# Optimization experiments

Measured on AMD Instinct MI355X. Metric: run time of the kernel, lower is better.

## Reference

```python
import jax, jax.numpy as jnp
import numpy as np
from jax import lax

WIN = 11
SIGMA = 1.5
C1 = 0.01 ** 2
C2 = 0.03 ** 2


def _gauss_window(c):
    x = np.arange(WIN) - WIN // 2
    g = np.exp(-(x ** 2) / (2.0 * SIGMA ** 2))
    g = g / g.sum()
    w2d = np.outer(g, g).astype(np.float32)  # [11,11]
    return jnp.asarray(np.broadcast_to(w2d, (c, 1, WIN, WIN)).copy())


def _dwconv(x, kernel, groups):
    # x: [B,C,H,W], kernel: [C,1,kh,kw] depthwise, stride 1, SAME padding
    return lax.conv_general_dilated(
        x, kernel, window_strides=(1, 1), padding='SAME',
        dimension_numbers=('NCHW', 'OIHW', 'NCHW'),
        feature_group_count=groups)


_SOBEL_X = jnp.asarray(np.array([[-1, 0, 1], [-2, 0, 2], [-1, 0, 1]], np.float32))
_SOBEL_Y = jnp.asarray(np.array([[1, 2, 1], [0, 0, 0], [-1, -2, -1]], np.float32))


def _sobel_xy(x):
    # x: [B,3,H,W] -> depthwise 3x3 sobel on each channel (same as per-channel conv2d)
    c = x.shape[1]
    kx = jnp.broadcast_to(_SOBEL_X, (c, 1, 3, 3))
    ky = jnp.broadcast_to(_SOBEL_Y, (c, 1, 3, 3))
    return _dwconv(x, kx, c), _dwconv(x, ky, c)


def _rgb2ycrcb(im):
    R, G, B = im[:, 0:1], im[:, 1:2], im[:, 2:3]
    Y = 0.299 * R + 0.587 * G + 0.114 * B
    Cr = (R - Y) * 0.713 + 0.5
    Cb = (B - Y) * 0.564 + 0.5
    return Y, Cr, Cb


def _ssim(img1, img2, channel):
    w = _gauss_window(channel)
    mu1 = _dwconv(img1, w, channel)
    mu2 = _dwconv(img2, w, channel)
    mu1_sq = mu1 * mu1
    mu2_sq = mu2 * mu2
    mu12 = mu1 * mu2
    s1 = _dwconv(img1 * img1, w, channel) - mu1_sq
    s2 = _dwconv(img2 * img2, w, channel) - mu2_sq
    s12 = _dwconv(img1 * img2, w, channel) - mu12
    ssim_map = ((2 * mu12 + C1) * (2 * s12 + C2)) / ((mu1_sq + mu2_sq + C1) * (s1 + s2 + C2))
    return ssim_map.mean()


def _l1(a, b):
    return jnp.mean(jnp.abs(a - b))


def setup_inputs() -> dict:
    key = jax.random.key(0)
    k1, k2, k3 = jax.random.split(key, 3)
    shp = (16, 3, 512, 512)
    return {
        'input_vis': jax.random.uniform(k1, shp, jnp.float32),
        'input_ir': jax.random.uniform(k2, shp, jnp.float32),
        'fuse': jax.random.uniform(k3, shp, jnp.float32),
    }


def reference(input_vis, input_ir, fuse):
    # color components
    _, Cr_F, Cb_F = _rgb2ycrcb(fuse)
    _, Cr_V, Cb_V = _rgb2ycrcb(input_vis)
    Y_ir = input_ir[:, 0:1]

    # sobel gradients (depthwise over 3 channels == per-channel conv + cat)
    Fgx, Fgy = _sobel_xy(fuse)
    Vgx, Vgy = _sobel_xy(input_vis)
    Igx, Igy = _sobel_xy(input_ir)
    joint_gx = jnp.maximum(Vgx, Igx)
    joint_gy = jnp.maximum(Vgy, Igy)
    joint_int = jnp.maximum(input_vis, input_ir)

    con_loss = _l1(fuse, joint_int)
    gradient_loss = 0.5 * _l1(Fgx, joint_gx) + 0.5 * _l1(Fgy, joint_gy)
    color_loss = _l1(Cb_F, Cb_V) + _l1(Cr_F, Cr_V)

    # SSIM: rgb-vs-fused (3ch) and ir-Y vs gray(fused) (1ch)
    ssim_rgb = _ssim(input_vis, fuse, 3)
    gray_fused = (0.2989 * fuse[:, 0:1] + 0.587 * fuse[:, 1:2] + 0.114 * fuse[:, 2:3])
    ssim_ir = _ssim(Y_ir, gray_fused, 1)
    ssim_loss = 1.0 - (ssim_rgb + ssim_ir) / 2.0

    return 0.5 * con_loss + 0.2 * gradient_loss + 1.0 * color_loss + 0.1 * ssim_loss
```

## Files before the change

kernel.cpp:

```cpp
#include <hip/hip_runtime.h>

#define IMG_H 512
#define IMG_W 512
#define CH_STRIDE (IMG_H*IMG_W)
#define IMG_STRIDE (3*CH_STRIDE)

using f4    = __attribute__((ext_vector_type(4))) float;
using h4    = __attribute__((ext_vector_type(4))) _Float16;
using h8    = __attribute__((ext_vector_type(8))) _Float16;
using f32x4 = __attribute__((ext_vector_type(4))) float;

#define NSLOT 64
#define SLOT_F 32

__global__ __launch_bounds__(256) void k_zero(float* __restrict__ acc) {
  int i = threadIdx.x;
  *(f4*)&acc[i*8]     = f4{0,0,0,0};
  *(f4*)&acc[i*8 + 4] = f4{0,0,0,0};
}

__device__ __forceinline__ float block_sum(float v, float* red) {
  #pragma unroll
  for (int o = 32; o > 0; o >>= 1) v += __shfl_down(v, o, 64);
  __syncthreads();
  if ((threadIdx.x & 63) == 0) red[threadIdx.x >> 6] = v;
  __syncthreads();
  return red[0] + red[1] + red[2] + red[3];
}

__device__ __forceinline__ h4 cvt4(f4 v) {
  return h4{(_Float16)v.x,(_Float16)v.y,(_Float16)v.z,(_Float16)v.w};
}
__device__ __forceinline__ h8 zero8() {
  return h8{(_Float16)0,(_Float16)0,(_Float16)0,(_Float16)0,
            (_Float16)0,(_Float16)0,(_Float16)0,(_Float16)0};
}

#define R1W 68
#define R1N (18*R1W)

#define SXW 88
#define SXH 26
#define SF_STRIDE (SXH*SXW)
#define HB_OFF    (2*SF_STRIDE)
#define HB_F      (64*32)
#define SMEM_H    (HB_OFF + 4*HB_F)
#define SMEM_BYTES (SMEM_H*2 + 128)

#define N_SSIM 8192

__device__ __forceinline__ void phaseB(_Float16* S, h8 bh,
                                       int lr, int lg, int xo) {
  const int px = xo + lr;
  const int sgrp = (px ^ (px >> 2)) & 3;
  #pragma unroll
  for (int rt = 0; rt < 2; ++rt) {
    int row_s = rt*16 + lr;
    int rcl = row_s > 25 ? 25 : row_s;
    int rbase = rcl*SXW + xo + lg*8;
    h8 a = *(const h8*)&S[rbase];
    h8 b = *(const h8*)&S[SF_STRIDE + rbase];
    if (row_s > 25) { a = zero8(); b = zero8(); }
    h8 p = a*a + b*b;
    h8 q = a*b;
    f32x4 d0 = __builtin_amdgcn_mfma_f32_16x16x32_f16(
                   a, bh, f32x4{0.f,0.f,0.f,0.f}, 0, 0, 0);
    f32x4 d1 = __builtin_amdgcn_mfma_f32_16x16x32_f16(
                   b, bh, f32x4{0.f,0.f,0.f,0.f}, 0, 0, 0);
    f32x4 d2 = __builtin_amdgcn_mfma_f32_16x16x32_f16(
                   p, bh, f32x4{0.f,0.f,0.f,0.f}, 0, 0, 0);
    f32x4 d3 = __builtin_amdgcn_mfma_f32_16x16x32_f16(
                   q, bh, f32x4{0.f,0.f,0.f,0.f}, 0, 0, 0);
    int k0 = rt*16 + lg*4;
    int bb2 = k0 << 1;
    int sbk = ((((bb2 >> 4) ^ sgrp) << 4) | (bb2 & 15));
    int base = HB_OFF + px*32 + (sbk >> 1);
    h4 h0, h1, h2c, h3;
    #pragma unroll
    for (int r2 = 0; r2 < 4; ++r2) {
      h0[r2]  = (_Float16)d0[r2];
      h1[r2]  = (_Float16)d1[r2];
      h2c[r2] = (_Float16)d2[r2];
      h3[r2]  = (_Float16)d3[r2];
    }
    *(h4*)&S[base + 0*HB_F] = h0;
    *(h4*)&S[base + 1*HB_F] = h1;
    *(h4*)&S[base + 2*HB_F] = h2c;
    *(h4*)&S[base + 3*HB_F] = h3;
  }
}

__device__ __forceinline__ float phaseC(const _Float16* S, h8 bv,
                                        int lr, int lg, int xo) {
  const int pxA = xo + lr;
  const int sgrp = (pxA ^ (pxA >> 2)) & 3;
  const int gi = lg ^ sgrp;
  f32x4 dd[4];
  #pragma unroll
  for (int f = 0; f < 4; ++f) {
    h8 a = *(const h8*)&S[HB_OFF + f*HB_F + pxA*32 + gi*8];
    dd[f] = __builtin_amdgcn_mfma_f32_16x16x32_f16(
                a, bv, f32x4{0.f,0.f,0.f,0.f}, 0, 0, 0);
  }
  float ss = 0.f;
  #pragma unroll
  for (int r2 = 0; r2 < 4; ++r2) {
    float mu1 = dd[0][r2], mu2 = dd[1][r2];
    float sP  = dd[2][r2], sQ  = dd[3][r2];
    float mu12 = mu1*mu2, mss = mu1*mu1 + mu2*mu2;
    float s12 = sQ - mu12, sps = sP - mss;
    ss += ((2.f*mu12 + 1e-4f)*(2.f*s12 + 9e-4f)) /
          ((mss + 1e-4f)*(sps + 9e-4f));
  }
  return ss;
}

__global__ __launch_bounds__(256, 4) void k_main(
    const float* __restrict__ vis, const float* __restrict__ ir,
    const float* __restrict__ fuse, float* __restrict__ acc)
{
  __shared__ __align__(16) char smem[SMEM_BYTES];
  float* red = (float*)(smem + SMEM_H*2);
  const int tid = threadIdx.x;
  const int bid = blockIdx.x;
  float* aslot = acc + (bid & (NSLOT-1))*SLOT_F;

  if (bid < N_SSIM) {
    const int z = bid >> 7;
    const int n = z >> 2, pair = z & 3;
    const int x0 = (bid & 7)*64;
    const int y0a = ((bid >> 3) & 15)*32;
    const int y0b = y0a + 16;
    _Float16* S = (_Float16*)smem;

    const int lr = tid & 15;
    const int lg = (tid >> 4) & 3;
    const int wvw = tid >> 6;
    const int xo = wvw*16;

    const float* xb;
    const float* yb;
    if (pair < 3) {
      xb = vis  + (n*3 + pair)*CH_STRIDE;
      yb = fuse + (n*3 + pair)*CH_STRIDE;
    } else {
      xb = ir   + n*IMG_STRIDE;
      yb = fuse + n*IMG_STRIDE;
    }

    h8 bh, bv;
    #pragma unroll
    for (int e = 0; e < 8; ++e) {
      int k = lg*8 + e;
      int jh = k - lr - 3;
      int jv = k - lr;
      float wh = 0.f, wvv = 0.f;
      if ((unsigned)jh < 11u) {
        float d = (float)(jh - 5);
        wh = exp2f(-d*d*0.32059889798f) * 0.26601255681f;
      }
      if ((unsigned)jv < 11u) {
        float d = (float)(jv - 5);
        wvv = exp2f(-d*d*0.32059889798f) * 0.26601255681f;
      }
      bh[e] = (_Float16)wh;
      bv[e] = (_Float16)wvv;
    }

    const int row0 = tid / 20,        k0c = tid - row0*20;
    const int i1r  = tid + 256;
    const int row1 = i1r / 20,        k1c = i1r - row1*20;

    if (pair < 3) {
      for (int i = tid; i < SXH*20; i += 256) {
        int row = i / 20, k = i - row*20;
        int gy = y0a - 5 + row, gx = x0 - 8 + 4*k;
        f4 xv = {0,0,0,0}, yv = {0,0,0,0};
        if ((unsigned)gy < IMG_H && (unsigned)gx < IMG_W) {
          int off = gy*IMG_W + gx;
          xv = *(const f4*)&xb[off];
          yv = *(const f4*)&yb[off];
        }
        int ib = row*SXW + 4*k;
        *(h4*)&S[ib]             = cvt4(xv);
        *(h4*)&S[SF_STRIDE + ib] = cvt4(yv);
      }
    } else {
      for (int i = tid; i < SXH*20; i += 256) {
        int row = i / 20, k = i - row*20;
        int gy = y0a - 5 + row, gx = x0 - 8 + 4*k;
        f4 xv = {0,0,0,0}, yv = {0,0,0,0};
        if ((unsigned)gy < IMG_H && (unsigned)gx < IMG_W) {
          int off = gy*IMG_W + gx;
          xv = *(const f4*)&xb[off];
          f4 rr = *(const f4*)&yb[off];
          f4 gg = *(const f4*)&yb[off + CH_STRIDE];
          f4 bb = *(const f4*)&yb[off + 2*CH_STRIDE];
          #pragma unroll
          for (int j = 0; j < 4; ++j)
            yv[j] = 0.2989f*rr[j] + 0.587f*gg[j] + 0.114f*bb[j];
        }
        int ib = row*SXW + 4*k;
        *(h4*)&S[ib]             = cvt4(xv);
        *(h4*)&S[SF_STRIDE + ib] = cvt4(yv);
      }
    }
    __syncthreads();

    f4 p0x = {0,0,0,0}, p0y = {0,0,0,0}, p1x = {0,0,0,0}, p1y = {0,0,0,0};
    f4 q0g = {0,0,0,0}, q0b = {0,0,0,0}, q1g = {0,0,0,0}, q1b = {0,0,0,0};
    {
      int gy0 = y0b - 5 + row0, gx0 = x0 - 8 + 4*k0c;
      int gy1 = y0b - 5 + row1, gx1 = x0 - 8 + 4*k1c;
      bool v0 = (unsigned)gy0 < IMG_H && (unsigned)gx0 < IMG_W;
      bool v1 = (unsigned)gy1 < IMG_H && (unsigned)gx1 < IMG_W;
      int o0 = gy0*IMG_W + gx0, o1 = gy1*IMG_W + gx1;
      if (pair < 3) {
        if (v0) { p0x = *(const f4*)&xb[o0]; p0y = *(const f4*)&yb[o0]; }
        if (v1) { p1x = *(const f4*)&xb[o1]; p1y = *(const f4*)&yb[o1]; }
      } else {
        if (v0) {
          p0x = *(const f4*)&xb[o0];
          p0y = *(const f4*)&yb[o0];
          q0g = *(const f4*)&yb[o0 + CH_STRIDE];
          q0b = *(const f4*)&yb[o0 + 2*CH_STRIDE];
        }
        if (v1) {
          p1x = *(const f4*)&xb[o1];
          p1y = *(const f4*)&yb[o1];
          q1g = *(const f4*)&yb[o1 + CH_STRIDE];
          q1b = *(const f4*)&yb[o1 + 2*CH_STRIDE];
        }
      }
    }

    phaseB(S, bh, lr, lg, xo);
    __syncthreads();

    {
      int ib0 = row0*SXW + 4*k0c;
      int ib1 = row1*SXW + 4*k1c;
      if (pair < 3) {
        *(h4*)&S[ib0]             = cvt4(p0x);
        *(h4*)&S[SF_STRIDE + ib0] = cvt4(p0y);
        *(h4*)&S[ib1]             = cvt4(p1x);
        *(h4*)&S[SF_STRIDE + ib1] = cvt4(p1y);
      } else {
        f4 l0, l1;
        #pragma unroll
        for (int j = 0; j < 4; ++j) {
          l0[j] = 0.2989f*p0y[j] + 0.587f*q0g[j] + 0.114f*q0b[j];
          l1[j] = 0.2989f*p1y[j] + 0.587f*q1g[j] + 0.114f*q1b[j];
        }
        *(h4*)&S[ib0]             = cvt4(p0x);
        *(h4*)&S[SF_STRIDE + ib0] = cvt4(l0);
        *(h4*)&S[ib1]             = cvt4(p1x);
        *(h4*)&S[SF_STRIDE + ib1] = cvt4(l1);
      }
      if (tid < 8) {
        int k2 = tid + 12;
        int gy2 = y0b + 20, gx2 = x0 - 8 + 4*k2;
        f4 xv = {0,0,0,0}, yv = {0,0,0,0};
        if ((unsigned)gy2 < IMG_H && (unsigned)gx2 < IMG_W) {
          int off = gy2*IMG_W + gx2;
          xv = *(const f4*)&xb[off];
          if (pair < 3) yv = *(const f4*)&yb[off];
          else {
            f4 rr = *(const f4*)&yb[off];
            f4 gg = *(const f4*)&yb[off + CH_STRIDE];
            f4 bb = *(const f4*)&yb[off + 2*CH_STRIDE];
            #pragma unroll
            for (int j = 0; j < 4; ++j)
              yv[j] = 0.2989f*rr[j] + 0.587f*gg[j] + 0.114f*bb[j];
          }
        }
        int ib2 = 25*SXW + 4*k2;
        *(h4*)&S[ib2]             = cvt4(xv);
        *(h4*)&S[SF_STRIDE + ib2] = cvt4(yv);
      }
    }

    float ss = phaseC(S, bv, lr, lg, xo);
    __syncthreads();
    phaseB(S, bh, lr, lg, xo);
    __syncthreads();
    ss += phaseC(S, bv, lr, lg, xo);

    #pragma unroll
    for (int o = 32; o > 0; o >>= 1) ss += __shfl_down(ss, o, 64);
    if ((tid & 63) == 0) atomicAdd(&aslot[(pair == 3) ? 6 : 5], ss);

  } else {
    const int r = bid - N_SSIM;
    const int x0 = (r & 7)*64;
    const int y0 = ((r >> 3) & 31)*16;
    const int n  = r >> 8;
    float* s = (float*)smem;
    const int ox = (tid & 15)*4;
    const int oy = tid >> 4;

    float con=0.f, gxs=0.f, gys=0.f, cbs=0.f, crs=0.f;
    float pv[3][4], pf[3][4];

    for (int c = 0; c < 3; ++c) {
      const float* pv0 = vis  + (n*3 + c)*CH_STRIDE;
      const float* pi0 = ir   + (n*3 + c)*CH_STRIDE;
      const float* pf0 = fuse + (n*3 + c)*CH_STRIDE;
      for (int i = tid; i < 864; i += 256) {
        int f = i / 288;
        int rr = i - f*288;
        int row = rr >> 4, k = rr & 15;
        int gy = y0 - 1 + row, gx = x0 + 4*k;
        f4 v = {0,0,0,0};
        const float* bp = (f == 0) ? pv0 : ((f == 1) ? pi0 : pf0);
        if ((unsigned)gy < IMG_H) v = *(const f4*)&bp[gy*IMG_W + gx];
        float* dst = s + f*R1N + row*R1W + 1 + 4*k;
        dst[0]=v.x; dst[1]=v.y; dst[2]=v.z; dst[3]=v.w;
      }
      if (tid < 108) {
        int f = tid / 36;
        int rr = tid - f*36;
        int row = rr >> 1, side = rr & 1;
        int gy = y0 - 1 + row;
        int gx = side ? (x0 + 64) : (x0 - 1);
        float v = 0.f;
        const float* bp = (f == 0) ? pv0 : ((f == 1) ? pi0 : pf0);
        if ((unsigned)gx < IMG_W && (unsigned)gy < IMG_H) v = bp[gy*IMG_W + gx];
        s[f*R1N + row*R1W + (side ? 65 : 0)] = v;
      }
      __syncthreads();

      float cen[3][4], gxv[3][4], gyv[3][4];
      #pragma unroll
      for (int t = 0; t < 3; ++t) {
        const float* sf = s + t*R1N;
        float r0[8], r1[8], r2[8];
        {
          f4 a = *(const f4*)&sf[(oy+0)*R1W + ox], b = *(const f4*)&sf[(oy+0)*R1W + ox + 4];
          r0[0]=a.x; r0[1]=a.y; r0[2]=a.z; r0[3]=a.w; r0[4]=b.x; r0[5]=b.y; r0[6]=b.z; r0[7]=b.w;
        }
        {
          f4 a = *(const f4*)&sf[(oy+1)*R1W + ox], b = *(const f4*)&sf[(oy+1)*R1W + ox + 4];
          r1[0]=a.x; r1[1]=a.y; r1[2]=a.z; r1[3]=a.w; r1[4]=b.x; r1[5]=b.y; r1[6]=b.z; r1[7]=b.w;
        }
        {
          f4 a = *(const f4*)&sf[(oy+2)*R1W + ox], b = *(const f4*)&sf[(oy+2)*R1W + ox + 4];
          r2[0]=a.x; r2[1]=a.y; r2[2]=a.z; r2[3]=a.w; r2[4]=b.x; r2[5]=b.y; r2[6]=b.z; r2[7]=b.w;
        }
        #pragma unroll
        for (int j = 0; j < 4; ++j) {
          gxv[t][j] = (r0[j+2]-r0[j]) + 2.f*(r1[j+2]-r1[j]) + (r2[j+2]-r2[j]);
          gyv[t][j] = (r0[j] + 2.f*r0[j+1] + r0[j+2]) - (r2[j] + 2.f*r2[j+1] + r2[j+2]);
          cen[t][j] = r1[j+1];
        }
      }
      #pragma unroll
      for (int j = 0; j < 4; ++j) {
        con += fabsf(cen[2][j] - fmaxf(cen[0][j], cen[1][j]));
        gxs += fabsf(gxv[2][j] - fmaxf(gxv[0][j], gxv[1][j]));
        gys += fabsf(gyv[2][j] - fmaxf(gyv[0][j], gyv[1][j]));
        pv[c][j] = cen[0][j];
        pf[c][j] = cen[2][j];
      }
      __syncthreads();
    }

    #pragma unroll
    for (int j = 0; j < 4; ++j) {
      float Yf = 0.299f*pf[0][j] + 0.587f*pf[1][j] + 0.114f*pf[2][j];
      float Yv = 0.299f*pv[0][j] + 0.587f*pv[1][j] + 0.114f*pv[2][j];
      crs += fabsf(0.713f*((pf[0][j]-Yf) - (pv[0][j]-Yv)));
      cbs += fabsf(0.564f*((pf[2][j]-Yf) - (pv[2][j]-Yv)));
    }

    float r0 = block_sum(con, red);
    float r1 = block_sum(gxs, red);
    float r2 = block_sum(gys, red);
    float r3 = block_sum(cbs, red);
    float r4 = block_sum(crs, red);
    if (tid == 0) {
      atomicAdd(&aslot[0], r0);
      atomicAdd(&aslot[1], r1);
      atomicAdd(&aslot[2], r2);
      atomicAdd(&aslot[3], r3);
      atomicAdd(&aslot[4], r4);
    }
  }
}

__global__ __launch_bounds__(64) void k_final(
    const float* __restrict__ acc, float* __restrict__ out)
{
  int lane = threadIdx.x;
  float s[7];
  #pragma unroll
  for (int c = 0; c < 7; ++c) {
    float x = acc[lane*SLOT_F + c];
    #pragma unroll
    for (int o = 32; o > 0; o >>= 1) x += __shfl_down(x, o, 64);
    s[c] = x;
  }
  if (lane == 0) {
    const float N3 = 16.f*3.f*512.f*512.f;
    const float N1 = 16.f*512.f*512.f;
    float con_loss  = s[0] / N3;
    float grad_loss = 0.5f*(s[1]/N3) + 0.5f*(s[2]/N3);
    float color_loss = s[3]/N1 + s[4]/N1;
    float ssim_loss = 1.f - (s[5]/N3 + s[6]/N1)*0.5f;
    out[0] = 0.5f*con_loss + 0.2f*grad_loss + color_loss + 0.1f*ssim_loss;
  }
}

extern "C" void kernel_launch(void* const* d_in, const int* in_sizes, int n_in,
                              void* d_out, int out_size, void* d_ws, size_t ws_size,
                              hipStream_t stream) {
  (void)in_sizes; (void)n_in; (void)out_size; (void)ws_size;
  const float* vis  = (const float*)d_in[0];
  const float* ir   = (const float*)d_in[1];
  const float* fuse = (const float*)d_in[2];
  float* out = (float*)d_out;
  float* acc = (float*)d_ws;

  k_zero<<<dim3(1,1,1), dim3(256,1,1), 0, stream>>>(acc);
  k_main<<<dim3(12288,1,1), dim3(256,1,1), 0, stream>>>(vis, ir, fuse, acc);
  k_final<<<dim3(1,1,1), dim3(64,1,1), 0, stream>>>(acc, out);
}
```

Measured before the change: 236.1 us.

## Interleave SSIM and gradient blocks, precompute weight table, cheaper reductions

Block indices now interleave two SSIM tiles with one gradient/L1 tile in every group of three, replacing the old layout that ran all SSIM blocks before all L1 blocks. The goal is a better mix of compute-heavy and memory-heavy work across CUs. The Gaussian MFMA weight fragments are computed once in k_zero and stored in a table inside the accumulator buffer, so each SSIM block loads them instead of evaluating exp2. The division is replaced by a hardware reciprocal, the five block reductions are merged so they share one barrier, and the occupancy hint rises to 6. The changes add register pressure risk and slightly less precise division.

```diff
diff --git a/kernel.cpp b/kernel.cpp
--- a/kernel.cpp
+++ b/kernel.cpp
@@ -12,20 +12,36 @@
 
 #define NSLOT 64
 #define SLOT_F 32
+#define WTAB_OFF 8192
 
 __global__ __launch_bounds__(256) void k_zero(float* __restrict__ acc) {
   int i = threadIdx.x;
   *(f4*)&acc[i*8]     = f4{0,0,0,0};
   *(f4*)&acc[i*8 + 4] = f4{0,0,0,0};
-}
-
-__device__ __forceinline__ float block_sum(float v, float* red) {
-  #pragma unroll
-  for (int o = 32; o > 0; o >>= 1) v += __shfl_down(v, o, 64);
-  __syncthreads();
-  if ((threadIdx.x & 63) == 0) red[threadIdx.x >> 6] = v;
-  __syncthreads();
-  return red[0] + red[1] + red[2] + red[3];
+  if (i < 64) {
+    int lr = i & 15, lg = (i >> 4) & 3;
+    h8 bh, bv;
+    #pragma unroll
+    for (int e = 0; e < 8; ++e) {
+      int k = lg*8 + e;
+      int jh = k - lr - 3;
+      int jv = k - lr;
+      float wh = 0.f, wvv = 0.f;
+      if ((unsigned)jh < 11u) {
+        float d = (float)(jh - 5);
+        wh = exp2f(-d*d*0.32059889798f) * 0.26601255681f;
+      }
+      if ((unsigned)jv < 11u) {
+        float d = (float)(jv - 5);
+        wvv = exp2f(-d*d*0.32059889798f) * 0.26601255681f;
+      }
+      bh[e] = (_Float16)wh;
+      bv[e] = (_Float16)wvv;
+    }
+    char* wt = (char*)acc + WTAB_OFF + i*32;
+    *(h8*)wt        = bh;
+    *(h8*)(wt + 16) = bv;
+  }
 }
 
 __device__ __forceinline__ h4 cvt4(f4 v) {
@@ -46,8 +62,6 @@
 #define HB_F      (64*32)
 #define SMEM_H    (HB_OFF + 4*HB_F)
 #define SMEM_BYTES (SMEM_H*2 + 128)
-
-#define N_SSIM 8192
 
 __device__ __forceinline__ void phaseB(_Float16* S, h8 bh,
                                        int lr, int lg, int xo) {
@@ -109,13 +123,14 @@
     float sP  = dd[2][r2], sQ  = dd[3][r2];
     float mu12 = mu1*mu2, mss = mu1*mu1 + mu2*mu2;
     float s12 = sQ - mu12, sps = sP - mss;
-    ss += ((2.f*mu12 + 1e-4f)*(2.f*s12 + 9e-4f)) /
-          ((mss + 1e-4f)*(sps + 9e-4f));
+    float num = (2.f*mu12 + 1e-4f)*(2.f*s12 + 9e-4f);
+    float den = (mss + 1e-4f)*(sps + 9e-4f);
+    ss += num * __builtin_amdgcn_rcpf(den);
   }
   return ss;
 }
 
-__global__ __launch_bounds__(256, 4) void k_main(
+__global__ __launch_bounds__(256, 6) void k_main(
     const float* __restrict__ vis, const float* __restrict__ ir,
     const float* __restrict__ fuse, float* __restrict__ acc)
 {
@@ -125,11 +140,15 @@
   const int bid = blockIdx.x;
   float* aslot = acc + (bid & (NSLOT-1))*SLOT_F;
 
-  if (bid < N_SSIM) {
-    const int z = bid >> 7;
+  const int sb = bid / 3;
+  const int rm = bid - sb*3;
+
+  if (rm < 2) {
+    const int si = sb*2 + rm;
+    const int z = si >> 7;
     const int n = z >> 2, pair = z & 3;
-    const int x0 = (bid & 7)*64;
-    const int y0a = ((bid >> 3) & 15)*32;
+    const int x0 = (si & 7)*64;
+    const int y0a = ((si >> 3) & 15)*32;
     const int y0b = y0a + 16;
     _Float16* S = (_Float16*)smem;
 
@@ -149,22 +168,10 @@
     }
 
     h8 bh, bv;
-    #pragma unroll
-    for (int e = 0; e < 8; ++e) {
-      int k = lg*8 + e;
-      int jh = k - lr - 3;
-      int jv = k - lr;
-      float wh = 0.f, wvv = 0.f;
-      if ((unsigned)jh < 11u) {
-        float d = (float)(jh - 5);
-        wh = exp2f(-d*d*0.32059889798f) * 0.26601255681f;
-      }
-      if ((unsigned)jv < 11u) {
-        float d = (float)(jv - 5);
-        wvv = exp2f(-d*d*0.32059889798f) * 0.26601255681f;
-      }
-      bh[e] = (_Float16)wh;
-      bv[e] = (_Float16)wvv;
+    {
+      const char* wt = (const char*)acc + WTAB_OFF + (tid & 63)*32;
+      bh = *(const h8*)wt;
+      bv = *(const h8*)(wt + 16);
     }
 
     const int row0 = tid / 20,        k0c = tid - row0*20;
@@ -291,7 +298,7 @@
     if ((tid & 63) == 0) atomicAdd(&aslot[(pair == 3) ? 6 : 5], ss);
 
   } else {
-    const int r = bid - N_SSIM;
+    const int r = sb;
     const int x0 = (r & 7)*64;
     const int y0 = ((r >> 3) & 31)*16;
     const int n  = r >> 8;
@@ -373,18 +380,18 @@
       cbs += fabsf(0.564f*((pf[2][j]-Yf) - (pv[2][j]-Yv)));
     }
 
-    float r0 = block_sum(con, red);
-    float r1 = block_sum(gxs, red);
-    float r2 = block_sum(gys, red);
-    float r3 = block_sum(cbs, red);
-    float r4 = block_sum(crs, red);
-    if (tid == 0) {
-      atomicAdd(&aslot[0], r0);
-      atomicAdd(&aslot[1], r1);
-      atomicAdd(&aslot[2], r2);
-      atomicAdd(&aslot[3], r3);
-      atomicAdd(&aslot[4], r4);
-    }
+    float sums[5] = {con, gxs, gys, cbs, crs};
+    const int lane = tid & 63, wvw2 = tid >> 6;
+    #pragma unroll
+    for (int i2 = 0; i2 < 5; ++i2) {
+      float v = sums[i2];
+      #pragma unroll
+      for (int o = 32; o > 0; o >>= 1) v += __shfl_down(v, o, 64);
+      if (lane == 0) red[wvw2*5 + i2] = v;
+    }
+    __syncthreads();
+    if (tid < 5)
+      atomicAdd(&aslot[tid], red[tid] + red[5+tid] + red[10+tid] + red[15+tid]);
   }
 }
 
```

Measured after the change: 211.1 us. -10.6%, faster.
